# Kernel tuning notes

Hardware: AMD Instinct MI355X
Metric: run time of the kernel (lower is better)

Reference implementation:

```python
import jax, jax.numpy as jnp
import numpy as np

N = 20000      # nodes
E = 160000     # edges
F_IN = 128     # num_node_features
D = 128        # embedding_size (out_channels)
H = 4          # heads
NEG = 0.2      # GATv2Conv negative_slope
N_LAYERS = 3


def setup_inputs() -> dict:
    key = jax.random.key(0)
    ks = jax.random.split(key, 12)
    s = 0.05
    return {
        "x": jax.random.normal(ks[0], (N, F_IN), jnp.float32),
        "edge_index": jax.random.randint(ks[1], (2, E), 0, N, jnp.int64),
        "edge_attr": jax.random.normal(ks[2], (E, 2), jnp.float32),
        "Wf": jax.random.normal(ks[3], (F_IN, D), jnp.float32) * s,
        "bf": jnp.zeros((D,), jnp.float32),
        "Wl": jax.random.normal(ks[4], (D, H * D), jnp.float32) * s,
        "bl": jnp.zeros((H * D,), jnp.float32),
        "Wr": jax.random.normal(ks[5], (D, H * D), jnp.float32) * s,
        "br": jnp.zeros((H * D,), jnp.float32),
        "We": jax.random.normal(ks[6], (2, H * D), jnp.float32) * s,
        "att": jax.random.normal(ks[7], (H, D), jnp.float32) * s,
        "bias_out": jnp.zeros((D,), jnp.float32),
    }


def reference(x, edge_index, edge_attr, Wf, bf, Wl, bl, Wr, br, We, att, bias_out):
    src, dst = edge_index[0], edge_index[1]

    # add_self_loops with fill_value='mean': self-loop edge_attr = mean of
    # incoming edge_attr per node (0 where a node has no incoming edges)
    ea_sum = jax.ops.segment_sum(edge_attr, dst, num_segments=N)            # [N,2]
    cnt = jax.ops.segment_sum(jnp.ones((E,), edge_attr.dtype), dst, num_segments=N)
    loop_attr = ea_sum / jnp.maximum(cnt, 1.0)[:, None]
    loop_idx = jnp.arange(N, dtype=src.dtype)
    fsrc = jnp.concatenate([src, loop_idx])                                  # [E+N]
    fdst = jnp.concatenate([dst, loop_idx])
    fea = jnp.concatenate([edge_attr, loop_attr], axis=0)                    # [E+N,2]

    ee = (fea @ We).reshape(-1, H, D)                                        # [E+N,H,D]

    def gatv2_layer(h):
        xl = (h @ Wl + bl).reshape(N, H, D)   # lin_l -> source-side / message
        xr = (h @ Wr + br).reshape(N, H, D)   # lin_r -> target-side
        e = jax.nn.leaky_relu(xl[fsrc] + xr[fdst] + ee, NEG)                 # [E+N,H,D]
        logits = jnp.einsum('ehd,hd->eh', e, att)                            # [E+N,H]
        m = jax.ops.segment_max(logits, fdst, num_segments=N)                # [N,H]
        w = jnp.exp(logits - m[fdst])
        denom = jax.ops.segment_sum(w, fdst, num_segments=N)                 # [N,H]
        alpha = w / denom[fdst]                                              # segment softmax
        msg = xl[fsrc] * alpha[..., None]                                    # [E+N,H,D]
        out = jax.ops.segment_sum(msg, fdst, num_segments=N)                 # [N,H,D]
        return out.mean(axis=1) + bias_out                                   # concat=False

    h = x @ Wf + bf
    for _ in range(N_LAYERS):
        h = jax.nn.leaky_relu(gatv2_layer(h), 0.01)  # F.leaky_relu default slope
    return h
```

## Files before the change

### kernel.cpp

```cpp
#include <hip/hip_runtime.h>
#include <hip/hip_bf16.h>

#define NN 20000
#define NE 160000
#define EF (NE + NN)
#define DD 128
#define HH 4
#define NPA (NN * DD)
#define NPW (1024 * 128 + 128 * 128 + 1024)
#define DEGB ((NE + 255) / 256)

typedef unsigned short u16;
typedef unsigned int u32;

using short8  = __attribute__((ext_vector_type(8))) short;
using ushort8 = __attribute__((ext_vector_type(8))) unsigned short;
using float4v = __attribute__((ext_vector_type(4))) float;

__device__ __forceinline__ float bf2f(u16 u) {
    union { u32 i; float f; } c;
    c.i = ((u32)u) << 16;
    return c.f;
}
__device__ __forceinline__ u16 f2bf(float f) {
    union { float f; u32 u; } c;
    c.f = f;
    u32 u = c.u;
    u32 r = (u + 0x7fffu + ((u >> 16) & 1u)) >> 16;
    return (u16)r;
}


__global__ void k_zero_i(int* __restrict__ p, int n) {
    int i = blockIdx.x * blockDim.x + threadIdx.x;
    if (i < n) p[i] = 0;
}

__global__ void k_zero_f(float* __restrict__ p, int n) {
    int i = blockIdx.x * blockDim.x + threadIdx.x;
    if (i < n) p[i] = 0.f;
}


__global__ void k_degpack(const int* __restrict__ ei, const float* __restrict__ ea,
                          const float* __restrict__ x,
                          const float* __restrict__ Wl, const float* __restrict__ Wr,
                          const float* __restrict__ bl, const float* __restrict__ br,
                          const float* __restrict__ Wf,
                          int* __restrict__ cnt, float* __restrict__ ea_sum,
                          u16* __restrict__ Axh, u16* __restrict__ Axl,
                          u16* __restrict__ W2Th, u16* __restrict__ W2Tl,
                          u16* __restrict__ WfTh, u16* __restrict__ WfTl,
                          float* __restrict__ bias2) {
    int gb = blockIdx.x;
    if (gb < DEGB) {
        int e = gb * 256 + threadIdx.x;
        if (e >= NE) return;
        int t = ei[NE + e];
        atomicAdd(&cnt[t], 1);
        atomicAdd(&ea_sum[t * 2 + 0], ea[e * 2 + 0]);
        atomicAdd(&ea_sum[t * 2 + 1], ea[e * 2 + 1]);
        return;
    }
    int i = (gb - DEGB) * 256 + threadIdx.x;
    if (i < NPA) {
        float a = x[i];
        u16 h = f2bf(a);
        Axh[i] = h;
        Axl[i] = f2bf(a - bf2f(h));
        return;
    }
    i -= NPA;
    if (i < 1024 * 128) {
        int n = i >> 7, k = i & 127;
        float w = (n < 512) ? Wl[k * 512 + n] : Wr[k * 512 + (n - 512)];
        u16 h = f2bf(w);
        W2Th[n * 128 + k] = h;
        W2Tl[n * 128 + k] = f2bf(w - bf2f(h));
    } else if (i < 1024 * 128 + 128 * 128) {
        int u = i - 1024 * 128;
        int n = u >> 7, k = u & 127;
        float w = Wf[k * 128 + n];
        u16 h = f2bf(w);
        WfTh[n * 128 + k] = h;
        WfTl[n * 128 + k] = f2bf(w - bf2f(h));
    } else if (i < NPW) {
        int n = i - (1024 * 128 + 128 * 128);
        bias2[n] = (n < 512) ? bl[n] : br[n - 512];
    }
}


__global__ void k_scan(const int* __restrict__ cnt, int* __restrict__ rowptr) {
    __shared__ int wsum[16];
    __shared__ int s_base;
    int tid = threadIdx.x;
    int w = tid >> 6, l = tid & 63;
    if (tid == 0) { s_base = 0; rowptr[0] = 0; }
    __syncthreads();
    const int chunks = (NN + 1023) / 1024;
    for (int c = 0; c < chunks; ++c) {
        int i = c * 1024 + tid;
        int v = (i < NN) ? (cnt[i] + 1) : 0;
        #pragma unroll
        for (int off = 1; off < 64; off <<= 1) {
            int u = __shfl_up(v, off, 64);
            if (l >= off) v += u;
        }
        if (l == 63) wsum[w] = v;
        __syncthreads();
        if (w == 0) {
            int s = (l < 16) ? wsum[l] : 0;
            #pragma unroll
            for (int off = 1; off < 16; off <<= 1) {
                int u = __shfl_up(s, off, 64);
                if (l >= off) s += u;
            }
            if (l < 16) wsum[l] = s;
        }
        __syncthreads();
        int waveoff = (w > 0) ? wsum[w - 1] : 0;
        int incl = s_base + waveoff + v;
        if (i < NN) rowptr[i + 1] = incl;
        __syncthreads();
        if (tid == 1023) s_base = incl;
        __syncthreads();
    }
}


__global__ void k_fill(const int* __restrict__ ei, const float* __restrict__ ea,
                       const int* __restrict__ rowptr, int* __restrict__ fillc,
                       const int* __restrict__ cnt, const float* __restrict__ ea_sum,
                       int* __restrict__ srcs,
                       float* __restrict__ fa0, float* __restrict__ fa1) {
    int e = blockIdx.x * blockDim.x + threadIdx.x;
    if (e < NE) {
        int s = ei[e], t = ei[NE + e];
        int pos = atomicAdd(&fillc[t], 1);
        int slot = rowptr[t] + pos;
        srcs[slot] = s;
        fa0[slot] = ea[e * 2];
        fa1[slot] = ea[e * 2 + 1];
    } else if (e < NE + NN) {
        int n = e - NE;
        int slot = rowptr[n + 1] - 1;
        srcs[slot] = n;
        float c = fmaxf((float)cnt[n], 1.f);
        fa0[slot] = ea_sum[n * 2 + 0] / c;
        fa1[slot] = ea_sum[n * 2 + 1] / c;
    }
}


template<int SPLIT>
__global__ __launch_bounds__(256, 3) void k_mgemm(
        const u16* __restrict__ Ahg, const u16* __restrict__ Alg,
        const u16* __restrict__ BTh, const u16* __restrict__ BTl,
        const float* __restrict__ bias, float* __restrict__ C1,
        u16* __restrict__ C2b,
        u16* __restrict__ Oh, u16* __restrict__ Ol, int M) {
    __shared__ u16 sAh[64 * 128], sBh[64 * 128], sBl[64 * 128];
    int m0 = blockIdx.y * 64;
    int t = threadIdx.x;
    int lane = t & 63;
    int wm = (t >> 6) & 1;
    int wn = t >> 7;
    int fm = lane & 15;
    int q8 = (lane >> 4) * 8;

    short8 fal[4][2];
    #pragma unroll
    for (int i = 0; i < 2; ++i) {
        const u16* p = Alg + (size_t)(m0 + wm * 32 + i * 16 + fm) * 128 + q8;
        #pragma unroll
        for (int kk = 0; kk < 4; ++kk)
            fal[kk][i] = *(const short8*)(p + kk * 32);
    }

    #pragma unroll
    for (int i = 0; i < 4; ++i) {
        int c = t + 256 * i;
        int row = c >> 4, ch = c & 15;
        int gm = m0 + row;
        short8 va = {0, 0, 0, 0, 0, 0, 0, 0};
        if (gm < M) va = *(const short8*)&Ahg[gm * 128 + ch * 8];
        *(short8*)&sAh[row * 128 + ((ch ^ (row & 15)) << 3)] = va;
    }

    int cq = q8 >> 3;

    for (int bb = 0; bb < 2; ++bb) {
        int n0 = (blockIdx.x * 2 + bb) * 64;
        __syncthreads();
        #pragma unroll
        for (int i = 0; i < 4; ++i) {
            int c = t + 256 * i;
            int row = c >> 4, ch = c & 15;
            int gn = n0 + row;
            int d = row * 128 + ((ch ^ (row & 15)) << 3);
            *(short8*)&sBh[d] = *(const short8*)&BTh[gn * 128 + ch * 8];
            *(short8*)&sBl[d] = *(const short8*)&BTl[gn * 128 + ch * 8];
        }
        __syncthreads();

        float4v zz = {0.f, 0.f, 0.f, 0.f};
        float4v acc[2][2];
        acc[0][0] = zz; acc[0][1] = zz; acc[1][0] = zz; acc[1][1] = zz;

        #pragma unroll
        for (int k0 = 0; k0 < 128; k0 += 32) {
            int cl = (k0 >> 3) + cq;
            int sw = (cl ^ fm) << 3;
            short8 fah[2], fbh[2], fbl[2];
            #pragma unroll
            for (int i = 0; i < 2; ++i) {
                int mr = wm * 32 + i * 16 + fm;
                fah[i] = *(const short8*)&sAh[mr * 128 + sw];
                int nr = wn * 32 + i * 16 + fm;
                fbh[i] = *(const short8*)&sBh[nr * 128 + sw];
                fbl[i] = *(const short8*)&sBl[nr * 128 + sw];
            }
            #pragma unroll
            for (int i = 0; i < 2; ++i)
                #pragma unroll
                for (int j = 0; j < 2; ++j) {
                    acc[i][j] = __builtin_amdgcn_mfma_f32_16x16x32_bf16(fah[i], fbh[j], acc[i][j], 0, 0, 0);
                    acc[i][j] = __builtin_amdgcn_mfma_f32_16x16x32_bf16(fah[i], fbl[j], acc[i][j], 0, 0, 0);
                    acc[i][j] = __builtin_amdgcn_mfma_f32_16x16x32_bf16(fal[k0 >> 5][i], fbh[j], acc[i][j], 0, 0, 0);
                }
        }

        #pragma unroll
        for (int i = 0; i < 2; ++i) {
            #pragma unroll
            for (int j = 0; j < 2; ++j) {
                int gn = n0 + wn * 32 + j * 16 + fm;
                float bv = bias[gn];
                #pragma unroll
                for (int r = 0; r < 4; ++r) {
                    int gm = m0 + wm * 32 + i * 16 + (lane >> 4) * 4 + r;
                    if (gm < M) {
                        float v = acc[i][j][r] + bv;
                        if (SPLIT) {
                            u16 h = f2bf(v);
                            Oh[gm * 128 + gn] = h;
                            Ol[gm * 128 + gn] = f2bf(v - bf2f(h));
                        } else if (n0 < 512) {
                            C1[gm * 512 + gn] = v;
                        } else {
                            C2b[gm * 512 + gn - 512] = f2bf(v);
                        }
                    }
                }
            }
        }
    }
}


__global__ __launch_bounds__(256) void k_gat(
        const int* __restrict__ rowptr, const int* __restrict__ srcs,
        const float* __restrict__ fa0, const float* __restrict__ fa1,
        const float* __restrict__ xl, const u16* __restrict__ xr,
        const float* __restrict__ We, const float* __restrict__ att,
        const float* __restrict__ bias_out,
        u16* __restrict__ Oh, u16* __restrict__ Ol,
        float* __restrict__ outp, int last) {
    int n = blockIdx.x * 4 + (threadIdx.x >> 6);
    if (n >= NN) return;
    int l = threadIdx.x & 63;
    int d0 = l * 8;
    float xrv[8], we0[8], we1[8], atv[8];
    {
        ushort8 u = *reinterpret_cast<const ushort8*>(&xr[(size_t)n * 512 + d0]);
        #pragma unroll
        for (int k = 0; k < 8; ++k) xrv[k] = bf2f(u[k]);
        float4 a = *reinterpret_cast<const float4*>(&We[d0]);
        float4 b = *reinterpret_cast<const float4*>(&We[d0 + 4]);
        we0[0]=a.x; we0[1]=a.y; we0[2]=a.z; we0[3]=a.w;
        we0[4]=b.x; we0[5]=b.y; we0[6]=b.z; we0[7]=b.w;
        a = *reinterpret_cast<const float4*>(&We[512 + d0]);
        b = *reinterpret_cast<const float4*>(&We[512 + d0 + 4]);
        we1[0]=a.x; we1[1]=a.y; we1[2]=a.z; we1[3]=a.w;
        we1[4]=b.x; we1[5]=b.y; we1[6]=b.z; we1[7]=b.w;
        a = *reinterpret_cast<const float4*>(&att[d0]);
        b = *reinterpret_cast<const float4*>(&att[d0 + 4]);
        atv[0]=a.x; atv[1]=a.y; atv[2]=a.z; atv[3]=a.w;
        atv[4]=b.x; atv[5]=b.y; atv[6]=b.z; atv[7]=b.w;
    }
    int b0 = rowptr[n], b1 = rowptr[n + 1];
    float acc[8] = {0.f,0.f,0.f,0.f,0.f,0.f,0.f,0.f};
    float den = 0.f;
    int sNext = srcs[b0];
    for (int e = b0; e < b1; ++e) {
        int s = sNext;
        if (e + 1 < b1) sNext = srcs[e + 1];
        float f0 = fa0[e], f1 = fa1[e];
        const float* xlp = &xl[(size_t)s * 512 + d0];
        float4 a = *reinterpret_cast<const float4*>(xlp);
        float4 b = *reinterpret_cast<const float4*>(xlp + 4);
        float xv[8] = {a.x, a.y, a.z, a.w, b.x, b.y, b.z, b.w};
        float p = 0.f;
        #pragma unroll
        for (int k = 0; k < 8; ++k) {
            float v = xv[k] + xrv[k] + f0 * we0[k] + f1 * we1[k];
            v = v > 0.f ? v : 0.2f * v;
            p += v * atv[k];
        }
        p += __shfl_xor(p, 1, 64);
        p += __shfl_xor(p, 2, 64);
        p += __shfl_xor(p, 4, 64);
        p += __shfl_xor(p, 8, 64);
        float wt = __expf(p);
        den += wt;
        #pragma unroll
        for (int k = 0; k < 8; ++k) acc[k] += wt * xv[k];
    }
    float inv = 1.f / den;
    float val[8];
    #pragma unroll
    for (int k = 0; k < 8; ++k) {
        float v = acc[k] * inv;
        v += __shfl_xor(v, 16, 64);
        v += __shfl_xor(v, 32, 64);
        val[k] = v;
    }
    if (l < 16) {
        #pragma unroll
        for (int k = 0; k < 8; ++k) {
            float v = val[k] * 0.25f + bias_out[d0 + k];
            v = v > 0.f ? v : 0.01f * v;
            val[k] = v;
        }
        if (last) {
            #pragma unroll
            for (int k = 0; k < 8; ++k) outp[n * 128 + d0 + k] = val[k];
        } else {
            #pragma unroll
            for (int k = 0; k < 8; ++k) {
                u16 hv = f2bf(val[k]);
                Oh[n * 128 + d0 + k] = hv;
                Ol[n * 128 + d0 + k] = f2bf(val[k] - bf2f(hv));
            }
        }
    }
}


extern "C" void kernel_launch(void* const* d_in, const int* in_sizes, int n_in,
                              void* d_out, int out_size, void* d_ws, size_t ws_size,
                              hipStream_t stream) {
    size_t o = 0;
    auto alloc = [&](size_t bytes) { size_t cur = o; o += (bytes + 255) & ~(size_t)255; return cur; };
    size_t off_cnt    = alloc((size_t)NN * 4);
    size_t off_fillc  = alloc((size_t)NN * 4);
    size_t off_easum  = alloc((size_t)NN * 2 * 4);
    size_t off_rowptr = alloc((size_t)(NN + 1) * 4);
    size_t off_srcs   = alloc((size_t)EF * 4);
    size_t off_fa0    = alloc((size_t)EF * 4);
    size_t off_fa1    = alloc((size_t)EF * 4);
    size_t off_axh    = alloc((size_t)NN * DD * 2);
    size_t off_axl    = alloc((size_t)NN * DD * 2);
    size_t off_ah     = alloc((size_t)NN * DD * 2);
    size_t off_al     = alloc((size_t)NN * DD * 2);
    size_t off_xl     = alloc((size_t)NN * 512 * 4);
    size_t off_xr     = alloc((size_t)NN * 512 * 2);
    size_t off_w2th   = alloc((size_t)1024 * 128 * 2);
    size_t off_w2tl   = alloc((size_t)1024 * 128 * 2);
    size_t off_wfth   = alloc((size_t)128 * 128 * 2);
    size_t off_wftl   = alloc((size_t)128 * 128 * 2);
    size_t off_bias2  = alloc((size_t)1024 * 4);
    size_t need = o;

    bool ok = (n_in == 12) && d_ws != nullptr && ws_size >= need
           && out_size == NN * DD
           && in_sizes[0] == NN * DD && in_sizes[1] == 2 * NE
           && in_sizes[2] == NE * 2 && in_sizes[3] == 128 * 128
           && in_sizes[5] == 128 * 512 && in_sizes[9] == 2 * 512
           && in_sizes[10] == 4 * 128 && in_sizes[11] == 128;
    if (!ok) {
        k_zero_f<<<(NN * DD + 255) / 256, 256, 0, stream>>>((float*)d_out, NN * DD);
        return;
    }

    const float* x        = (const float*)d_in[0];
    const int*   ei       = (const int*)d_in[1];
    const float* ea       = (const float*)d_in[2];
    const float* Wf       = (const float*)d_in[3];
    const float* bf       = (const float*)d_in[4];
    const float* Wl       = (const float*)d_in[5];
    const float* bl       = (const float*)d_in[6];
    const float* Wr       = (const float*)d_in[7];
    const float* br       = (const float*)d_in[8];
    const float* We       = (const float*)d_in[9];
    const float* att      = (const float*)d_in[10];
    const float* bias_out = (const float*)d_in[11];

    char* base = (char*)d_ws;
    int*   cnt    = (int*)(base + off_cnt);
    int*   fillc  = (int*)(base + off_fillc);
    float* ea_sum = (float*)(base + off_easum);
    int*   rowptr = (int*)(base + off_rowptr);
    int*   srcs   = (int*)(base + off_srcs);
    float* fa0    = (float*)(base + off_fa0);
    float* fa1    = (float*)(base + off_fa1);
    u16*   Axh    = (u16*)(base + off_axh);
    u16*   Axl    = (u16*)(base + off_axl);
    u16*   Ah     = (u16*)(base + off_ah);
    u16*   Al     = (u16*)(base + off_al);
    float* xl     = (float*)(base + off_xl);
    u16*   xr     = (u16*)(base + off_xr);
    u16*   W2Th   = (u16*)(base + off_w2th);
    u16*   W2Tl   = (u16*)(base + off_w2tl);
    u16*   WfTh   = (u16*)(base + off_wfth);
    u16*   WfTl   = (u16*)(base + off_wftl);
    float* bias2  = (float*)(base + off_bias2);

    int zero_ints = (int)((off_easum + (size_t)NN * 2 * 4 - off_cnt) / 4);
    k_zero_i<<<(zero_ints + 255) / 256, 256, 0, stream>>>(cnt, zero_ints);

    int packb = (NPA + NPW + 255) / 256;
    k_degpack<<<DEGB + packb, 256, 0, stream>>>(ei, ea, x, Wl, Wr, bl, br, Wf,
                                                cnt, ea_sum, Axh, Axl,
                                                W2Th, W2Tl, WfTh, WfTl, bias2);
    k_scan<<<1, 1024, 0, stream>>>(cnt, rowptr);
    k_fill<<<(NE + NN + 255) / 256, 256, 0, stream>>>(ei, ea, rowptr, fillc,
                                                      cnt, ea_sum, srcs, fa0, fa1);

    const int MT = (NN + 63) / 64;
    k_mgemm<1><<<dim3(1, MT), 256, 0, stream>>>(Axh, Axl, WfTh, WfTl,
                                                bf, nullptr, nullptr, Ah, Al, NN);

    for (int layer = 0; layer < 3; ++layer) {
        k_mgemm<0><<<dim3(8, MT), 256, 0, stream>>>(Ah, Al, W2Th, W2Tl,
                                                    bias2, xl, xr, nullptr, nullptr, NN);
        int last = (layer == 2);
        k_gat<<<(NN + 3) / 4, 256, 0, stream>>>(rowptr, srcs, fa0, fa1, xl, xr,
                                                We, att, bias_out, Ah, Al,
                                                (float*)d_out, last);
    }
}
```

Before: 463.9 us.

## Parallelize row-pointer scan across blocks and widen GEMM column tiles per block

Replaces the single-block serial scan over 20000 node counts with a two-pass multi-block scan: 40 blocks compute local prefix sums, then a second kernel adds the block offsets. Separately, the layer GEMM now processes four 64-column tiles per block instead of two, halving the grid's x-dimension. This reuses the A tile held in shared memory and registers across more output columns. The trade-off is less block-level parallelism, about 1256 blocks instead of 2512.

Result: faster. 428.8 us (-7.6%).

```diff
diff --git a/kernel.cpp b/kernel.cpp
--- a/kernel.cpp
+++ b/kernel.cpp
@@ -9,6 +9,7 @@
 #define NPA (NN * DD)
 #define NPW (1024 * 128 + 128 * 128 + 1024)
 #define DEGB ((NE + 255) / 256)
+#define NBLK 40
 
 typedef unsigned short u16;
 typedef unsigned int u32;
@@ -91,41 +92,49 @@
 }
 
 
-__global__ void k_scan(const int* __restrict__ cnt, int* __restrict__ rowptr) {
-    __shared__ int wsum[16];
-    __shared__ int s_base;
+__global__ __launch_bounds__(512) void k_scan_a(const int* __restrict__ cnt,
+                                                int* __restrict__ rowptr,
+                                                int* __restrict__ bsum) {
+    __shared__ int ws[8];
     int tid = threadIdx.x;
-    int w = tid >> 6, l = tid & 63;
-    if (tid == 0) { s_base = 0; rowptr[0] = 0; }
+    int i = blockIdx.x * 512 + tid;
+    int l = tid & 63, w = tid >> 6;
+    int v = (i < NN) ? (cnt[i] + 1) : 0;
+    #pragma unroll
+    for (int off = 1; off < 64; off <<= 1) {
+        int u = __shfl_up(v, off, 64);
+        if (l >= off) v += u;
+    }
+    if (l == 63) ws[w] = v;
     __syncthreads();
-    const int chunks = (NN + 1023) / 1024;
-    for (int c = 0; c < chunks; ++c) {
-        int i = c * 1024 + tid;
-        int v = (i < NN) ? (cnt[i] + 1) : 0;
-        #pragma unroll
-        for (int off = 1; off < 64; off <<= 1) {
-            int u = __shfl_up(v, off, 64);
-            if (l >= off) v += u;
-        }
-        if (l == 63) wsum[w] = v;
-        __syncthreads();
-        if (w == 0) {
-            int s = (l < 16) ? wsum[l] : 0;
-            #pragma unroll
-            for (int off = 1; off < 16; off <<= 1) {
-                int u = __shfl_up(s, off, 64);
-                if (l >= off) s += u;
-            }
-            if (l < 16) wsum[l] = s;
-        }
-        __syncthreads();
-        int waveoff = (w > 0) ? wsum[w - 1] : 0;
-        int incl = s_base + waveoff + v;
-        if (i < NN) rowptr[i + 1] = incl;
-        __syncthreads();
-        if (tid == 1023) s_base = incl;
-        __syncthreads();
-    }
+    if (w == 0) {
+        int s = (l < 8) ? ws[l] : 0;
+        #pragma unroll
+        for (int off = 1; off < 8; off <<= 1) {
+            int u = __shfl_up(s, off, 64);
+            if (l >= off) s += u;
+        }
+        if (l < 8) ws[l] = s;
+    }
+    __syncthreads();
+    v += (w > 0) ? ws[w - 1] : 0;
+    if (i < NN) rowptr[i + 1] = v;
+    if (tid == 511) bsum[blockIdx.x] = v;
+}
+
+__global__ void k_scan_c(int* __restrict__ rowptr, const int* __restrict__ bsum) {
+    int l = threadIdx.x & 63;
+    int v = (l < NBLK) ? bsum[l] : 0;
+    #pragma unroll
+    for (int off = 1; off < 64; off <<= 1) {
+        int u = __shfl_up(v, off, 64);
+        if (l >= off) v += u;
+    }
+    int i = blockIdx.x * blockDim.x + threadIdx.x;
+    int j = i >> 9;
+    int off = (j > 0) ? __shfl(v, j - 1, 64) : 0;
+    if (i < NN) rowptr[i + 1] += off;
+    if (i == 0) rowptr[0] = 0;
 }
 
 
@@ -153,7 +162,7 @@
 }
 
 
-template<int SPLIT>
+template<int SPLIT, int NB>
 __global__ __launch_bounds__(256, 3) void k_mgemm(
         const u16* __restrict__ Ahg, const u16* __restrict__ Alg,
         const u16* __restrict__ BTh, const u16* __restrict__ BTl,
@@ -190,8 +199,8 @@
 
     int cq = q8 >> 3;
 
-    for (int bb = 0; bb < 2; ++bb) {
-        int n0 = (blockIdx.x * 2 + bb) * 64;
+    for (int bb = 0; bb < NB; ++bb) {
+        int n0 = (blockIdx.x * NB + bb) * 64;
         __syncthreads();
         #pragma unroll
         for (int i = 0; i < 4; ++i) {
@@ -357,6 +366,7 @@
     size_t off_fillc  = alloc((size_t)NN * 4);
     size_t off_easum  = alloc((size_t)NN * 2 * 4);
     size_t off_rowptr = alloc((size_t)(NN + 1) * 4);
+    size_t off_bsum   = alloc((size_t)NBLK * 4);
     size_t off_srcs   = alloc((size_t)EF * 4);
     size_t off_fa0    = alloc((size_t)EF * 4);
     size_t off_fa1    = alloc((size_t)EF * 4);
@@ -402,6 +412,7 @@
     int*   fillc  = (int*)(base + off_fillc);
     float* ea_sum = (float*)(base + off_easum);
     int*   rowptr = (int*)(base + off_rowptr);
+    int*   bsum   = (int*)(base + off_bsum);
     int*   srcs   = (int*)(base + off_srcs);
     float* fa0    = (float*)(base + off_fa0);
     float* fa1    = (float*)(base + off_fa1);
@@ -424,17 +435,18 @@
     k_degpack<<<DEGB + packb, 256, 0, stream>>>(ei, ea, x, Wl, Wr, bl, br, Wf,
                                                 cnt, ea_sum, Axh, Axl,
                                                 W2Th, W2Tl, WfTh, WfTl, bias2);
-    k_scan<<<1, 1024, 0, stream>>>(cnt, rowptr);
+    k_scan_a<<<NBLK, 512, 0, stream>>>(cnt, rowptr, bsum);
+    k_scan_c<<<(NN + 255) / 256, 256, 0, stream>>>(rowptr, bsum);
     k_fill<<<(NE + NN + 255) / 256, 256, 0, stream>>>(ei, ea, rowptr, fillc,
                                                       cnt, ea_sum, srcs, fa0, fa1);
 
     const int MT = (NN + 63) / 64;
-    k_mgemm<1><<<dim3(1, MT), 256, 0, stream>>>(Axh, Axl, WfTh, WfTl,
-                                                bf, nullptr, nullptr, Ah, Al, NN);
+    k_mgemm<1, 2><<<dim3(1, MT), 256, 0, stream>>>(Axh, Axl, WfTh, WfTl,
+                                                   bf, nullptr, nullptr, Ah, Al, NN);
 
     for (int layer = 0; layer < 3; ++layer) {
-        k_mgemm<0><<<dim3(8, MT), 256, 0, stream>>>(Ah, Al, W2Th, W2Tl,
-                                                    bias2, xl, xr, nullptr, nullptr, NN);
+        k_mgemm<0, 4><<<dim3(4, MT), 256, 0, stream>>>(Ah, Al, W2Th, W2Tl,
+                                                       bias2, xl, xr, nullptr, nullptr, NN);
         int last = (layer == 2);
         k_gat<<<(NN + 3) / 4, 256, 0, stream>>>(rowptr, srcs, fa0, fa1, xl, xr,
                                                 We, att, bias_out, Ah, Al,
```
